# Kernel tuning notes

Hardware: AMD Instinct MI355X
Metric: run time of the kernel (lower is better)

Reference implementation:

```python
import jax, jax.numpy as jnp
import numpy as np

NEG_SLOPE = 0.2
LN_EPS = 1e-5


def _gat(x, src, dst, ea, Wl, Wr, We, att, b, heads, ch, concat):
    # GATv2 conv with edge features (eval mode: dropout = identity).
    N = x.shape[0]
    xl = (x @ Wl).reshape(N, heads, ch)          # source transform (also skip output)
    xr = (x @ Wr).reshape(N, heads, ch)          # target transform
    ee = (ea @ We).reshape(ea.shape[0], heads, ch)
    g = jax.nn.leaky_relu(xl[src] + xr[dst] + ee, NEG_SLOPE)   # [E,H,C]
    score = jnp.einsum('ehc,hc->eh', g, att)                    # [E,H]
    # segment softmax over destination nodes
    smax = jax.ops.segment_max(score, dst, num_segments=N)
    ex = jnp.exp(score - smax[dst])
    den = jax.ops.segment_sum(ex, dst, num_segments=N)
    alpha = ex / (den[dst] + 1e-16)
    out = jax.ops.segment_sum(xl[src] * alpha[..., None], dst, num_segments=N)  # [N,H,C]
    out = out.reshape(N, heads * ch) if concat else out.mean(axis=1)
    return out + b, xl.reshape(N, heads * ch)


def setup_inputs() -> dict:
    B, N, E, F, ED = 4, 20000, 640000, 64, 16
    HID, H1 = 16, 8
    key = jax.random.key(0)
    ks = jax.random.split(key, 32)

    def p(k, shape, fan):
        return (jax.random.normal(k, shape, jnp.float32) / np.float32(np.sqrt(fan)))

    inp = {
        'x': jax.random.normal(ks[0], (B, N, F), jnp.float32),
        'edge_attr': jax.random.normal(ks[1], (B, E, ED), jnp.float32),
        'edge_index': jax.random.randint(ks[2], (B, 2, E), 0, N, jnp.int32),
        # conv1: in=64, heads=8, out=16, concat
        'c1_Wl': p(ks[3], (F, H1 * HID), F),
        'c1_Wr': p(ks[4], (F, H1 * HID), F),
        'c1_We': p(ks[5], (ED, H1 * HID), ED),
        'c1_att': p(ks[6], (H1, HID), HID),
        'c1_b': jnp.zeros((H1 * HID,), jnp.float32),
        # conv2: in=128, heads=1, out=16, mean
        'c2_Wl': p(ks[7], (H1 * HID, HID), H1 * HID),
        'c2_Wr': p(ks[8], (H1 * HID, HID), H1 * HID),
        'c2_We': p(ks[9], (ED, HID), ED),
        'c2_att': p(ks[10], (1, HID), HID),
        'c2_b': jnp.zeros((HID,), jnp.float32),
        # skip_conv: in=128, heads=1, out=16, mean
        's_Wl': p(ks[11], (H1 * HID, HID), H1 * HID),
        's_Wr': p(ks[12], (H1 * HID, HID), H1 * HID),
        's_We': p(ks[13], (ED, HID), ED),
        's_att': p(ks[14], (1, HID), HID),
        's_b': jnp.zeros((HID,), jnp.float32),
        # lin_skip_conv + LayerNorm(16)
        'lin_W': p(ks[15], (HID, HID), HID),
        'lin_b': jnp.zeros((HID,), jnp.float32),
        'ln_g': jnp.ones((HID,), jnp.float32),
        'ln_b': jnp.zeros((HID,), jnp.float32),
    }
    return inp


def reference(x, edge_attr, edge_index,
              c1_Wl, c1_Wr, c1_We, c1_att, c1_b,
              c2_Wl, c2_Wr, c2_We, c2_att, c2_b,
              s_Wl, s_Wr, s_We, s_att, s_b,
              lin_W, lin_b, ln_g, ln_b):
    def single(xg, eig, eag):
        src, dst = eig[0], eig[1]
        h, skip = _gat(xg, src, dst, eag, c1_Wl, c1_Wr, c1_We, c1_att, c1_b, 8, 16, True)
        hx = jax.nn.elu(h)                                   # [N,128]
        x1, _ = _gat(hx, src, dst, eag, c2_Wl, c2_Wr, c2_We, c2_att, c2_b, 1, 16, False)
        # skip conv consumes hx with the residual skip features from conv1
        x2, _ = _gat(hx + skip, src, dst, eag, s_Wl, s_Wr, s_We, s_att, s_b, 1, 16, False)
        x2 = x2 @ lin_W.T + lin_b
        y = x1 + x2                                          # [N,16]
        mu = y.mean(-1, keepdims=True)
        var = ((y - mu) ** 2).mean(-1, keepdims=True)
        return (y - mu) / jnp.sqrt(var + LN_EPS) * ln_g + ln_b
    return jax.vmap(single)(x, edge_index, edge_attr)
```

## Files before the change

kernel.cpp:

```cpp
#include <hip/hip_runtime.h>
#include <hip/hip_bf16.h>

typedef __hip_bfloat16 bf16;
typedef float f32x2 __attribute__((ext_vector_type(2)));

#define NB_B 4
#define N 20000
#define E 640000
#define F 64
#define HC 128
#define ED 16
#define CH 16
#define NT 32

__device__ __forceinline__ float clampf(float v, float lo, float hi){ return fminf(fmaxf(v, lo), hi); }
__device__ __forceinline__ float ldv(const float* p, size_t i){ return p[i]; }
__device__ __forceinline__ float ldv(const bf16*  p, size_t i){ return __bfloat162float(p[i]); }
__device__ __forceinline__ void  stv(float* p, size_t i, float v){ p[i] = v; }
__device__ __forceinline__ void  stv(bf16*  p, size_t i, float v){ p[i] = __float2bfloat16(v); }
__device__ __forceinline__ unsigned short tobf(float v){ bf16 b = __float2bfloat16(v); return *(unsigned short*)&b; }
__device__ __forceinline__ float unpl(unsigned u){ return __uint_as_float(u << 16); }
__device__ __forceinline__ float unph(unsigned u){ return __uint_as_float(u & 0xffff0000u); }
__device__ __forceinline__ f32x2 mk2(float a, float b){ f32x2 r; r.x = a; r.y = b; return r; }
__device__ __forceinline__ int rfl(int v){ return __builtin_amdgcn_readfirstlane(v); }

#define L2E 1.44269504f

__device__ __forceinline__ float rsum16(float x){
  x += __int_as_float(__builtin_amdgcn_update_dpp(0, __float_as_int(x), 0x128, 0xf, 0xf, true));
  x += __int_as_float(__builtin_amdgcn_update_dpp(0, __float_as_int(x), 0x124, 0xf, 0xf, true));
  x += __int_as_float(__builtin_amdgcn_update_dpp(0, __float_as_int(x), 0x122, 0xf, 0xf, true));
  x += __int_as_float(__builtin_amdgcn_update_dpp(0, __float_as_int(x), 0x121, 0xf, 0xf, true));
  return x;
}

__global__ __launch_bounds__(256) void k_detect(const unsigned short* __restrict__ xu, int* __restrict__ flag){
  __shared__ int cnt[256];
  int tid = threadIdx.x;
  unsigned short lo = xu[2*tid];
  bf16 h = *(const bf16*)&lo;
  float v = fabsf(__bfloat162float(h));
  cnt[tid] = (v > 1e4f || (v != 0.f && v < 1e-4f)) ? 1 : 0;
  __syncthreads();
  for (int s=128; s>0; s>>=1){ if (tid<s) cnt[tid]+=cnt[tid+s]; __syncthreads(); }
  if (tid==0) *flag = (cnt[0] > 64) ? 1 : 0;
}

__global__ __launch_bounds__(256) void k_hist(const int* __restrict__ ei, int* __restrict__ cnt, int b0){
  int z = blockIdx.z, b = b0 + z;
  int e = blockIdx.x*256 + threadIdx.x;
  int d = ei[((size_t)b*2+1)*E + e];
  atomicAdd(&cnt[z*N + d], 1);
}

__global__ __launch_bounds__(256) void k_scan(const int* __restrict__ cnt, int* __restrict__ rowptr,
                                              int* __restrict__ cursor){
  int z = blockIdx.z, tid = threadIdx.x;
  const int* c = cnt + (size_t)z*N;
  int* rp = rowptr + (size_t)z*(N+1);
  int* cu = cursor + (size_t)z*N;
  const int CHK = (N + 255)/256;
  int lo = tid*CHK; int hi = lo + CHK; if (hi > N) hi = N; if (lo > N) lo = N;
  int s = 0;
  for (int i=lo;i<hi;i++) s += c[i];
  __shared__ int buf[256];
  buf[tid] = s; __syncthreads();
  for (int off=1; off<256; off<<=1){
    int t = (tid>=off) ? buf[tid-off] : 0;
    __syncthreads();
    buf[tid] += t;
    __syncthreads();
  }
  int run = buf[tid] - s;
  for (int i=lo;i<hi;i++){ int v=c[i]; rp[i]=run; cu[i]=run; run += v; }
  if (tid==255) rp[N] = run;
}

template<typename T>
__device__ __forceinline__ void scatter_body(const int* ei, int* cursor, int* csr,
                                             const T* ea, float* eacsr, int b0){
  int z = blockIdx.z, b = b0 + z;
  int e = blockIdx.x*256 + threadIdx.x;
  int s = ei[((size_t)b*2+0)*E + e];
  int d = ei[((size_t)b*2+1)*E + e];
  int pos = atomicAdd(&cursor[z*N + d], 1);
  csr[(size_t)z*E + pos] = s;
  float4* dst = (float4*)(eacsr + ((size_t)z*E + pos)*ED);
  const T* sp = ea + ((size_t)b*E + e)*ED;
  #pragma unroll
  for (int g=0; g<4; g++){
    float4 t;
    t.x = ldv(sp, g*4+0); t.y = ldv(sp, g*4+1); t.z = ldv(sp, g*4+2); t.w = ldv(sp, g*4+3);
    dst[g] = t;
  }
}
__global__ __launch_bounds__(256) void k_scatter(const int* ei, int* cursor, int* csr,
    const void* ea, float* eacsr, const int* flag, int b0){
  if (*flag) scatter_body(ei, cursor, csr, (const float*)ea, eacsr, b0);
  else       scatter_body(ei, cursor, csr, (const bf16*) ea, eacsr, b0);
}

template<typename T>
__device__ __forceinline__ void node1_body(const T* x, const T* Wl, const T* Wr,
                                           unsigned* xl1p, unsigned* xr1p, int b0,
                                           float (*xs)[F+4]){
  int z = blockIdx.z, b = b0 + z;
  int node0 = blockIdx.x*NT;
  for (int i=threadIdx.x; i<NT*F; i+=256){
    int n = i>>6, k = i&63;
    xs[n][k] = ldv(x, ((size_t)b*N + node0 + n)*F + k);
  }
  __syncthreads();
  int mat = threadIdx.x >> 7, c = threadIdx.x & 127;
  const T* W = mat ? Wr : Wl;
  float acc[NT];
  #pragma unroll
  for (int n=0;n<NT;n++) acc[n]=0.f;
  for (int k=0;k<F;k+=4){
    float w0 = ldv(W, (size_t)(k+0)*HC + c);
    float w1 = ldv(W, (size_t)(k+1)*HC + c);
    float w2 = ldv(W, (size_t)(k+2)*HC + c);
    float w3 = ldv(W, (size_t)(k+3)*HC + c);
    #pragma unroll
    for (int n=0;n<NT;n++){
      float4 xv = *(const float4*)&xs[n][k];
      acc[n] += xv.x*w0 + xv.y*w1 + xv.z*w2 + xv.w*w3;
    }
  }
  unsigned short* outp = (unsigned short*)(mat ? xr1p : xl1p);
  int half = c>>6, cc = c&63;
  #pragma unroll
  for (int n=0;n<NT;n++){
    float v = clampf(acc[n], -1e4f, 1e4f);
    outp[(((size_t)z*N + node0 + n)*64 + cc)*2 + half] = tobf(v);
  }
}
__global__ __launch_bounds__(256) void k_node1(const void* x, const void* Wl, const void* Wr,
    unsigned* xl1p, unsigned* xr1p, const int* flag, int b0){
  __shared__ float xs[NT][F+4];
  if (*flag) node1_body((const float*)x,(const float*)Wl,(const float*)Wr,xl1p,xr1p,b0,xs);
  else       node1_body((const bf16*) x,(const bf16*) Wl,(const bf16*) Wr,xl1p,xr1p,b0,xs);
}

template<typename T>
__device__ __forceinline__ void gather1_body(const int* __restrict__ rowptr, const int* __restrict__ csr,
    const float* __restrict__ eacsr, const T* __restrict__ We, const T* __restrict__ att, const T* __restrict__ b1,
    const unsigned* __restrict__ xl1p, const unsigned* __restrict__ xr1p, float* __restrict__ hx, int b0){
  int z = blockIdx.z;
  int lane = threadIdx.x & 63;
  int node = rfl(blockIdx.x*4 + (threadIdx.x >> 6));
  int rs = rfl(rowptr[(size_t)z*(N+1) + node]);
  int re = rfl(rowptr[(size_t)z*(N+1) + node + 1]);
  f32x2 w[ED];
  #pragma unroll
  for (int j=0;j<ED;j++) w[j] = mk2(ldv(We,(size_t)j*HC+lane), ldv(We,(size_t)j*HC+lane+64));
  f32x2 attv = mk2(ldv(att,(size_t)lane)*L2E, ldv(att,(size_t)lane+64)*L2E);
  unsigned xru = xr1p[((size_t)z*N + node)*64 + lane];
  f32x2 xr2 = mk2(unpl(xru), unph(xru));
  f32x2 acc = mk2(0.f,0.f), den = mk2(0.f,0.f);
  const unsigned* __restrict__ xlp = xl1p + (size_t)z*N*64;
  const int* __restrict__ csrz = csr + (size_t)z*E + rs;
  const float* __restrict__ eaz = eacsr + ((size_t)z*E + rs)*ED;
  int deg = re - rs;
  if (deg > 0){
    int s0 = rfl(csrz[0]);
    int s1 = (deg>1) ? rfl(csrz[1]) : s0;
    unsigned xa = xlp[(size_t)(unsigned)s0*64 + lane];
    unsigned xb = xlp[(size_t)(unsigned)s1*64 + lane];
    #pragma unroll 2
    for (int i=0;i<deg;i++){
      const float* __restrict__ ep = eaz + (size_t)i*ED;
      float ev[ED];
      #pragma unroll
      for (int j=0;j<ED;j++) ev[j] = ep[j];
      unsigned xw = xa;
      xa = xb;
      if (i+2 < deg){
        int sn = rfl(csrz[i+2]);
        xb = xlp[(size_t)(unsigned)sn*64 + lane];
      }
      f32x2 xl = mk2(unpl(xw), unph(xw));
      f32x2 g0 = xl + xr2, g1 = mk2(0.f,0.f);
      #pragma unroll
      for (int j=0;j<ED;j+=2){ g0 += w[j]*ev[j]; g1 += w[j+1]*ev[j+1]; }
      f32x2 g = g0 + g1;
      f32x2 lr;
      lr.x = fmaxf(g.x,0.f) + 0.2f*fminf(g.x,0.f);
      lr.y = fmaxf(g.y,0.f) + 0.2f*fminf(g.y,0.f);
      f32x2 v = lr*attv;
      float vL = rsum16(v.x);
      float vH = rsum16(v.y);
      f32x2 ex = mk2(exp2f(clampf(vL,-86.f,86.f)), exp2f(clampf(vH,-86.f,86.f)));
      den += ex;
      acc += ex*xl;
    }
  }
  float hL = acc.x/(den.x + 1e-16f) + ldv(b1,(size_t)lane);
  float hH = acc.y/(den.y + 1e-16f) + ldv(b1,(size_t)lane+64);
  hL = hL>0.f ? hL : expm1f(hL);
  hH = hH>0.f ? hH : expm1f(hH);
  hx[((size_t)z*N + node)*HC + lane]      = hL;
  hx[((size_t)z*N + node)*HC + lane + 64] = hH;
}
__global__ __launch_bounds__(256) void k_gather1(const int* __restrict__ rowptr, const int* __restrict__ csr,
    const float* __restrict__ eacsr,
    const void* We, const void* att, const void* b1,
    const unsigned* __restrict__ xl1p, const unsigned* __restrict__ xr1p, float* __restrict__ hx,
    const int* __restrict__ flag, int b0){
  if (*flag) gather1_body(rowptr,csr,eacsr,(const float*)We,(const float*)att,(const float*)b1,xl1p,xr1p,hx,b0);
  else       gather1_body(rowptr,csr,eacsr,(const bf16*) We,(const bf16*) att,(const bf16*) b1,xl1p,xr1p,hx,b0);
}

template<typename T>
__device__ __forceinline__ void node2_body(const float* hx, const unsigned* xl1p,
    const T* W2l, const T* W2r, const T* W3l, const T* W3r,
    unsigned* xl23p, unsigned* xr23p, int b0,
    float (*hv)[HC+4], float (*sv)[HC+4]){
  int z = blockIdx.z;
  int node0 = blockIdx.x*NT;
  for (int i=threadIdx.x; i<NT*HC; i+=256){
    int n = i>>7, k = i&127;
    float h = hx[((size_t)z*N + node0 + n)*HC + k];
    unsigned wxl = xl1p[((size_t)z*N + node0 + n)*64 + (k&63)];
    float xv = (k<64) ? unpl(wxl) : unph(wxl);
    hv[n][k] = h;
    sv[n][k] = h + xv;
  }
  __syncthreads();
  int o = threadIdx.x & 63;
  int mat = o >> 4, c = o & 15;
  int g = threadIdx.x >> 6;
  const T* W = (mat==0)? W2l : (mat==1)? W2r : (mat==2)? W3l : W3r;
  float (*src)[HC+4] = (mat<2)? hv : sv;
  float acc[8];
  #pragma unroll
  for (int j=0;j<8;j++) acc[j]=0.f;
  for (int k=0;k<HC;k+=4){
    float w0 = ldv(W, (size_t)(k+0)*CH + c);
    float w1 = ldv(W, (size_t)(k+1)*CH + c);
    float w2 = ldv(W, (size_t)(k+2)*CH + c);
    float w3 = ldv(W, (size_t)(k+3)*CH + c);
    #pragma unroll
    for (int j=0;j<8;j++){
      float4 xv = *(const float4*)&src[g*8+j][k];
      acc[j] += xv.x*w0 + xv.y*w1 + xv.z*w2 + xv.w*w3;
    }
  }
  unsigned short* arr = (unsigned short*)((mat&1) ? xr23p : xl23p);
  int half = mat>>1;
  #pragma unroll
  for (int j=0;j<8;j++){
    float v = clampf(acc[j], -1e4f, 1e4f);
    arr[(((size_t)z*N + node0 + g*8 + j)*CH + c)*2 + half] = tobf(v);
  }
}
__global__ __launch_bounds__(256) void k_node2(const float* hx, const unsigned* xl1p,
    const void* W2l, const void* W2r, const void* W3l, const void* W3r,
    unsigned* xl23p, unsigned* xr23p, const int* flag, int b0){
  __shared__ float hv[NT][HC+4];
  __shared__ float sv[NT][HC+4];
  if (*flag) node2_body(hx,xl1p,(const float*)W2l,(const float*)W2r,(const float*)W3l,(const float*)W3r,xl23p,xr23p,b0,hv,sv);
  else       node2_body(hx,xl1p,(const bf16*) W2l,(const bf16*) W2r,(const bf16*) W3l,(const bf16*) W3r,xl23p,xr23p,b0,hv,sv);
}

template<typename T>
__device__ __forceinline__ void gather23_body(const int* __restrict__ rowptr, const int* __restrict__ csr,
    const float* __restrict__ eacsr,
    const T* __restrict__ We2, const T* __restrict__ We3, const T* __restrict__ att2, const T* __restrict__ att3,
    const T* __restrict__ b2, const T* __restrict__ b3, const T* __restrict__ linW, const T* __restrict__ linb,
    const T* __restrict__ lng, const T* __restrict__ lnb,
    const unsigned* __restrict__ xl23p, const unsigned* __restrict__ xr23p,
    T* __restrict__ out, int b0){
  int z = blockIdx.z;
  int lane = threadIdx.x & 63;
  int g = lane >> 4, c = lane & 15;
  int node = rfl(blockIdx.x*4 + (threadIdx.x >> 6));
  int rs = rfl(rowptr[(size_t)z*(N+1) + node]);
  int re = rfl(rowptr[(size_t)z*(N+1) + node + 1]);
  int deg = re - rs;
  f32x2 w[ED];
  #pragma unroll
  for (int j=0;j<ED;j++) w[j] = mk2(ldv(We2,(size_t)j*CH+c), ldv(We3,(size_t)j*CH+c));
  f32x2 attv = mk2(ldv(att2,(size_t)c)*L2E, ldv(att3,(size_t)c)*L2E);
  unsigned xru = xr23p[((size_t)z*N + node)*CH + c];
  f32x2 xr2 = mk2(unpl(xru), unph(xru));
  f32x2 acc = mk2(0.f,0.f), den = mk2(0.f,0.f);
  const unsigned* __restrict__ xlp = xl23p + (size_t)z*N*CH;
  const int* __restrict__ csrz = csr + (size_t)z*E + rs;
  const float* __restrict__ eaz = eacsr + ((size_t)z*E + rs)*ED;
  if (deg > 0){
    int idx0 = (g < deg) ? g : deg-1;
    int s = csrz[idx0];
    unsigned xw = xlp[(size_t)(unsigned)s*CH + c];
    const float4* p0 = (const float4*)(eaz + (size_t)idx0*ED);
    float4 e0 = p0[0], e1 = p0[1], e2 = p0[2], e3 = p0[3];
    for (int i=0;i<deg;i+=4){
      bool act = (i + g) < deg;
      unsigned xcur = xw;
      float4 c0 = e0, c1 = e1, c2 = e2, c3 = e3;
      if (i+4 < deg){
        int ii = i + 4 + g;
        int idx = (ii < deg) ? ii : deg-1;
        int s2 = csrz[idx];
        xw = xlp[(size_t)(unsigned)s2*CH + c];
        const float4* p2 = (const float4*)(eaz + (size_t)idx*ED);
        e0 = p2[0]; e1 = p2[1]; e2 = p2[2]; e3 = p2[3];
      }
      float ev[ED];
      *(float4*)&ev[0]  = c0;
      *(float4*)&ev[4]  = c1;
      *(float4*)&ev[8]  = c2;
      *(float4*)&ev[12] = c3;
      f32x2 xl = mk2(unpl(xcur), unph(xcur));
      f32x2 g0 = xl + xr2, g1 = mk2(0.f,0.f);
      #pragma unroll
      for (int j=0;j<ED;j+=2){ g0 += w[j]*ev[j]; g1 += w[j+1]*ev[j+1]; }
      f32x2 gg = g0 + g1;
      f32x2 lr;
      lr.x = fmaxf(gg.x,0.f) + 0.2f*fminf(gg.x,0.f);
      lr.y = fmaxf(gg.y,0.f) + 0.2f*fminf(gg.y,0.f);
      f32x2 v = lr*attv;
      float v2 = rsum16(v.x);
      float v3 = rsum16(v.y);
      float x2e = exp2f(clampf(v2,-86.f,86.f));
      float x3e = exp2f(clampf(v3,-86.f,86.f));
      if (!act){ x2e = 0.f; x3e = 0.f; }
      f32x2 ex = mk2(x2e, x3e);
      den += ex;
      acc += ex*xl;
    }
  }
  acc.x += __shfl_xor(acc.x, 16); acc.x += __shfl_xor(acc.x, 32);
  acc.y += __shfl_xor(acc.y, 16); acc.y += __shfl_xor(acc.y, 32);
  den.x += __shfl_xor(den.x, 16); den.x += __shfl_xor(den.x, 32);
  den.y += __shfl_xor(den.y, 16); den.y += __shfl_xor(den.y, 32);
  float x1 = acc.x/(den.x + 1e-16f) + ldv(b2,(size_t)c);
  float x3 = acc.y/(den.y + 1e-16f) + ldv(b3,(size_t)c);
  float x2 = 0.f;
  #pragma unroll
  for (int j=0;j<16;j++) x2 += __shfl(x3, j, 16) * ldv(linW, (size_t)c*16 + j);
  x2 += ldv(linb,(size_t)c);
  float y = clampf(x1, -1e6f, 1e6f) + clampf(x2, -1e6f, 1e6f);
  float mu = rsum16(y)*(1.f/16.f);
  float dv = y - mu;
  float var = rsum16(dv*dv)*(1.f/16.f);
  float o = dv*rsqrtf(var + 1e-5f)*ldv(lng,(size_t)c) + ldv(lnb,(size_t)c);
  if (lane < 16) stv(out, ((size_t)(b0+z)*N + node)*16 + c, o);
}
__global__ __launch_bounds__(256) void k_gather23(const int* __restrict__ rowptr, const int* __restrict__ csr,
    const float* __restrict__ eacsr,
    const void* We2, const void* We3, const void* att2, const void* att3,
    const void* b2, const void* b3, const void* linW, const void* linb, const void* lng, const void* lnb,
    const unsigned* __restrict__ xl23p, const unsigned* __restrict__ xr23p,
    void* out, const int* __restrict__ flag, int b0){
  if (*flag) gather23_body(rowptr,csr,eacsr,(const float*)We2,(const float*)We3,(const float*)att2,(const float*)att3,
                           (const float*)b2,(const float*)b3,(const float*)linW,(const float*)linb,(const float*)lng,(const float*)lnb,
                           xl23p,xr23p,(float*)out,b0);
  else       gather23_body(rowptr,csr,eacsr,(const bf16*) We2,(const bf16*) We3,(const bf16*) att2,(const bf16*) att3,
                           (const bf16*) b2,(const bf16*) b3,(const bf16*) linW,(const bf16*) linb,(const bf16*) lng,(const bf16*) lnb,
                           xl23p,xr23p,(bf16*) out,b0);
}

struct WSP {
  int* flag;
  int *cnt, *cursor, *rowptr; int* csr;
  float *eacsr, *hx;
  unsigned *xl1p,*xr1p,*xl23p,*xr23p;
  size_t total;
};
static WSP mkws(char* base, int nb){
  WSP w; size_t off = 0;
  auto A = [&](size_t bytes)->char*{ char* p = base ? base + off : (char*)0; off = (off + bytes + 255) & ~(size_t)255; return p; };
  w.flag   = (int*)     A(256);
  w.cnt    = (int*)     A((size_t)nb*N*4);
  w.cursor = (int*)     A((size_t)nb*N*4);
  w.rowptr = (int*)     A((size_t)nb*(N+1)*4);
  w.csr    = (int*)     A((size_t)nb*E*4);
  w.eacsr  = (float*)   A((size_t)nb*E*ED*4);
  w.hx     = (float*)   A((size_t)nb*N*HC*4);
  w.xl1p   = (unsigned*)A((size_t)nb*N*64*4);
  w.xr1p   = (unsigned*)A((size_t)nb*N*64*4);
  w.xl23p  = (unsigned*)A((size_t)nb*N*CH*4);
  w.xr23p  = (unsigned*)A((size_t)nb*N*CH*4);
  w.total = off;
  return w;
}

extern "C" void kernel_launch(void* const* d_in, const int* in_sizes, int n_in,
                              void* d_out, int out_size, void* d_ws, size_t ws_size,
                              hipStream_t stream){
  const void* x    = d_in[0];
  const void* ea   = d_in[1];
  const int*  ei   = (const int*)d_in[2];
  const void* c1Wl = d_in[3], *c1Wr = d_in[4], *c1We = d_in[5];
  const void* c1att= d_in[6], *c1b  = d_in[7];
  const void* c2Wl = d_in[8], *c2Wr = d_in[9], *c2We = d_in[10];
  const void* c2att= d_in[11],*c2b  = d_in[12];
  const void* sWl  = d_in[13],*sWr  = d_in[14],*sWe  = d_in[15];
  const void* satt = d_in[16],*sb   = d_in[17];
  const void* linW = d_in[18],*linb = d_in[19];
  const void* lng  = d_in[20],*lnb  = d_in[21];

  auto run = [&](int b0, int nb){
    WSP w = mkws((char*)d_ws, nb);
    hipMemsetAsync(w.cnt, 0, (size_t)nb*N*4, stream);
    k_hist   <<<dim3(E/256,1,nb),   256,0,stream>>>(ei, w.cnt, b0);
    k_scan   <<<dim3(1,1,nb),       256,0,stream>>>(w.cnt, w.rowptr, w.cursor);
    k_scatter<<<dim3(E/256,1,nb),   256,0,stream>>>(ei, w.cursor, w.csr, ea, w.eacsr, w.flag, b0);
    k_node1  <<<dim3(N/NT,1,nb),    256,0,stream>>>(x, c1Wl, c1Wr, w.xl1p, w.xr1p, w.flag, b0);
    k_gather1<<<dim3(N/4,1,nb),     256,0,stream>>>(w.rowptr, w.csr, w.eacsr, c1We, c1att, c1b,
                                                    w.xl1p, w.xr1p, w.hx, w.flag, b0);
    k_node2  <<<dim3(N/NT,1,nb),    256,0,stream>>>(w.hx, w.xl1p, c2Wl, c2Wr, sWl, sWr,
                                                    w.xl23p, w.xr23p, w.flag, b0);
    k_gather23<<<dim3(N/4,1,nb),    256,0,stream>>>(w.rowptr, w.csr, w.eacsr, c2We, sWe, c2att, satt,
                                                    c2b, sb, linW, linb, lng, lnb,
                                                    w.xl23p, w.xr23p, d_out, w.flag, b0);
  };

  {
    WSP w0 = mkws((char*)d_ws, 1);
    k_detect<<<1,256,0,stream>>>((const unsigned short*)x, w0.flag);
  }

  WSP probe = mkws((char*)0, NB_B);
  if (ws_size >= probe.total){
    run(0, NB_B);
  } else {
    for (int g=0; g<NB_B; ++g) run(g, 1);
  }
}
```

Before: 1.214 ms.

## Restructure gather23 to one node per 16-lane group with LDS edge staging

The second gather kernel moves from one node per wavefront, with four edges processed in parallel per lane group, to one node per 16-lane group. Each group stages chunks of source indices and edge attributes in shared memory, then walks its edges with two-deep prefetch of source features, which removes the cross-group shuffle reduction. The first gather kernel is manually unrolled by two, loads edge attributes as float2 pairs, and both kernels use a branchless leaky-ReLU. The risk is load imbalance, since four nodes with different degrees now share a wavefront. The new path also relies on lockstep visibility of shared memory within a wave, with no barrier.

Result: faster. 1.141 ms (-6.0%).

```diff
diff --git a/kernel.cpp b/kernel.cpp
--- a/kernel.cpp
+++ b/kernel.cpp
@@ -12,6 +12,7 @@
 #define ED 16
 #define CH 16
 #define NT 32
+#define TB2 16
 
 __device__ __forceinline__ float clampf(float v, float lo, float hi){ return fminf(fmaxf(v, lo), hi); }
 __device__ __forceinline__ float ldv(const float* p, size_t i){ return p[i]; }
@@ -32,6 +33,10 @@
   x += __int_as_float(__builtin_amdgcn_update_dpp(0, __float_as_int(x), 0x122, 0xf, 0xf, true));
   x += __int_as_float(__builtin_amdgcn_update_dpp(0, __float_as_int(x), 0x121, 0xf, 0xf, true));
   return x;
+}
+__device__ __forceinline__ float leaky(float g){
+  float a = __uint_as_float(__float_as_uint(g) & 0x7fffffffu);
+  return fmaf(0.4f, a, 0.6f*g);
 }
 
 __global__ __launch_bounds__(256) void k_detect(const unsigned short* __restrict__ xu, int* __restrict__ flag){
@@ -154,46 +159,49 @@
   f32x2 w[ED];
   #pragma unroll
   for (int j=0;j<ED;j++) w[j] = mk2(ldv(We,(size_t)j*HC+lane), ldv(We,(size_t)j*HC+lane+64));
-  f32x2 attv = mk2(ldv(att,(size_t)lane)*L2E, ldv(att,(size_t)lane+64)*L2E);
+  float attL = ldv(att,(size_t)lane)*L2E, attH = ldv(att,(size_t)lane+64)*L2E;
   unsigned xru = xr1p[((size_t)z*N + node)*64 + lane];
   f32x2 xr2 = mk2(unpl(xru), unph(xru));
   f32x2 acc = mk2(0.f,0.f), den = mk2(0.f,0.f);
   const unsigned* __restrict__ xlp = xl1p + (size_t)z*N*64;
   const int* __restrict__ csrz = csr + (size_t)z*E + rs;
-  const float* __restrict__ eaz = eacsr + ((size_t)z*E + rs)*ED;
+  const f32x2* __restrict__ eaz = (const f32x2*)(eacsr + ((size_t)z*E + rs)*ED);
   int deg = re - rs;
   if (deg > 0){
+    auto EDGE = [&](const f32x2* er, unsigned xw){
+      f32x2 xl = mk2(unpl(xw), unph(xw));
+      f32x2 g0 = xl + xr2, g1 = mk2(0.f,0.f);
+      #pragma unroll
+      for (int jp=0;jp<8;jp++){ g0 += w[2*jp]*er[jp].x; g1 += w[2*jp+1]*er[jp].y; }
+      f32x2 g = g0 + g1;
+      float vL = rsum16(leaky(g.x)*attL);
+      float vH = rsum16(leaky(g.y)*attH);
+      f32x2 ex = mk2(exp2f(clampf(vL,-86.f,86.f)), exp2f(clampf(vH,-86.f,86.f)));
+      den += ex;
+      acc += ex*xl;
+    };
     int s0 = rfl(csrz[0]);
     int s1 = (deg>1) ? rfl(csrz[1]) : s0;
     unsigned xa = xlp[(size_t)(unsigned)s0*64 + lane];
     unsigned xb = xlp[(size_t)(unsigned)s1*64 + lane];
-    #pragma unroll 2
-    for (int i=0;i<deg;i++){
-      const float* __restrict__ ep = eaz + (size_t)i*ED;
-      float ev[ED];
+    f32x2 eA[8], eB[8];
+    #pragma unroll
+    for (int p=0;p<8;p++) eA[p] = eaz[p];
+    int i = 0;
+    for (; i+1 < deg; i += 2){
       #pragma unroll
-      for (int j=0;j<ED;j++) ev[j] = ep[j];
-      unsigned xw = xa;
-      xa = xb;
+      for (int p=0;p<8;p++) eB[p] = eaz[(size_t)(i+1)*8 + p];
+      unsigned x0 = xa, x1 = xb;
+      if (i+2 < deg){ int sn = rfl(csrz[i+2]); xa = xlp[(size_t)(unsigned)sn*64 + lane]; }
+      if (i+3 < deg){ int sn = rfl(csrz[i+3]); xb = xlp[(size_t)(unsigned)sn*64 + lane]; }
+      EDGE(eA, x0);
       if (i+2 < deg){
-        int sn = rfl(csrz[i+2]);
-        xb = xlp[(size_t)(unsigned)sn*64 + lane];
+        #pragma unroll
+        for (int p=0;p<8;p++) eA[p] = eaz[(size_t)(i+2)*8 + p];
       }
-      f32x2 xl = mk2(unpl(xw), unph(xw));
-      f32x2 g0 = xl + xr2, g1 = mk2(0.f,0.f);
-      #pragma unroll
-      for (int j=0;j<ED;j+=2){ g0 += w[j]*ev[j]; g1 += w[j+1]*ev[j+1]; }
-      f32x2 g = g0 + g1;
-      f32x2 lr;
-      lr.x = fmaxf(g.x,0.f) + 0.2f*fminf(g.x,0.f);
-      lr.y = fmaxf(g.y,0.f) + 0.2f*fminf(g.y,0.f);
-      f32x2 v = lr*attv;
-      float vL = rsum16(v.x);
-      float vH = rsum16(v.y);
-      f32x2 ex = mk2(exp2f(clampf(vL,-86.f,86.f)), exp2f(clampf(vH,-86.f,86.f)));
-      den += ex;
-      acc += ex*xl;
+      EDGE(eB, x1);
     }
+    if (i < deg) EDGE(eA, xa);
   }
   float hL = acc.x/(den.x + 1e-16f) + ldv(b1,(size_t)lane);
   float hH = acc.y/(den.y + 1e-16f) + ldv(b1,(size_t)lane+64);
@@ -266,74 +274,68 @@
 template<typename T>
 __device__ __forceinline__ void gather23_body(const int* __restrict__ rowptr, const int* __restrict__ csr,
     const float* __restrict__ eacsr,
-    const T* __restrict__ We2, const T* __restrict__ We3, const T* __restrict__ att2, const T* __restrict__ att3,
-    const T* __restrict__ b2, const T* __restrict__ b3, const T* __restrict__ linW, const T* __restrict__ linb,
-    const T* __restrict__ lng, const T* __restrict__ lnb,
+    const T* We2, const T* We3, const T* att2, const T* att3,
+    const T* b2, const T* b3, const T* linW, const T* linb, const T* lng, const T* lnb,
     const unsigned* __restrict__ xl23p, const unsigned* __restrict__ xr23p,
-    T* __restrict__ out, int b0){
+    T* out, int b0, int (*ssrc)[TB2], float (*eas)[TB2][16]){
   int z = blockIdx.z;
-  int lane = threadIdx.x & 63;
-  int g = lane >> 4, c = lane & 15;
-  int node = rfl(blockIdx.x*4 + (threadIdx.x >> 6));
-  int rs = rfl(rowptr[(size_t)z*(N+1) + node]);
-  int re = rfl(rowptr[(size_t)z*(N+1) + node + 1]);
-  int deg = re - rs;
+  int slot = threadIdx.x >> 4;
+  int node = blockIdx.x*16 + slot;
+  int c = threadIdx.x & 15;
+  int rs = rowptr[(size_t)z*(N+1) + node];
+  int re = rowptr[(size_t)z*(N+1) + node + 1];
+  unsigned xru = xr23p[((size_t)z*N + node)*CH + c];
+  f32x2 xr2 = mk2(unpl(xru), unph(xru));
   f32x2 w[ED];
   #pragma unroll
   for (int j=0;j<ED;j++) w[j] = mk2(ldv(We2,(size_t)j*CH+c), ldv(We3,(size_t)j*CH+c));
   f32x2 attv = mk2(ldv(att2,(size_t)c)*L2E, ldv(att3,(size_t)c)*L2E);
-  unsigned xru = xr23p[((size_t)z*N + node)*CH + c];
-  f32x2 xr2 = mk2(unpl(xru), unph(xru));
   f32x2 acc = mk2(0.f,0.f), den = mk2(0.f,0.f);
   const unsigned* __restrict__ xlp = xl23p + (size_t)z*N*CH;
-  const int* __restrict__ csrz = csr + (size_t)z*E + rs;
-  const float* __restrict__ eaz = eacsr + ((size_t)z*E + rs)*ED;
-  if (deg > 0){
-    int idx0 = (g < deg) ? g : deg-1;
-    int s = csrz[idx0];
-    unsigned xw = xlp[(size_t)(unsigned)s*CH + c];
-    const float4* p0 = (const float4*)(eaz + (size_t)idx0*ED);
-    float4 e0 = p0[0], e1 = p0[1], e2 = p0[2], e3 = p0[3];
-    for (int i=0;i<deg;i+=4){
-      bool act = (i + g) < deg;
-      unsigned xcur = xw;
-      float4 c0 = e0, c1 = e1, c2 = e2, c3 = e3;
-      if (i+4 < deg){
-        int ii = i + 4 + g;
-        int idx = (ii < deg) ? ii : deg-1;
-        int s2 = csrz[idx];
-        xw = xlp[(size_t)(unsigned)s2*CH + c];
-        const float4* p2 = (const float4*)(eaz + (size_t)idx*ED);
-        e0 = p2[0]; e1 = p2[1]; e2 = p2[2]; e3 = p2[3];
-      }
-      float ev[ED];
-      *(float4*)&ev[0]  = c0;
-      *(float4*)&ev[4]  = c1;
-      *(float4*)&ev[8]  = c2;
-      *(float4*)&ev[12] = c3;
-      f32x2 xl = mk2(unpl(xcur), unph(xcur));
-      f32x2 g0 = xl + xr2, g1 = mk2(0.f,0.f);
-      #pragma unroll
-      for (int j=0;j<ED;j+=2){ g0 += w[j]*ev[j]; g1 += w[j+1]*ev[j+1]; }
-      f32x2 gg = g0 + g1;
-      f32x2 lr;
-      lr.x = fmaxf(gg.x,0.f) + 0.2f*fminf(gg.x,0.f);
-      lr.y = fmaxf(gg.y,0.f) + 0.2f*fminf(gg.y,0.f);
-      f32x2 v = lr*attv;
-      float v2 = rsum16(v.x);
-      float v3 = rsum16(v.y);
-      float x2e = exp2f(clampf(v2,-86.f,86.f));
-      float x3e = exp2f(clampf(v3,-86.f,86.f));
-      if (!act){ x2e = 0.f; x3e = 0.f; }
-      f32x2 ex = mk2(x2e, x3e);
-      den += ex;
-      acc += ex*xl;
+  const int* __restrict__ csrz = csr + (size_t)z*E;
+
+  auto edge = [&](int i, unsigned xw){
+    f32x2 xl = mk2(unpl(xw), unph(xw));
+    float ev[16];
+    const float4* er = (const float4*)eas[slot][i];
+    *(float4*)&ev[0]  = er[0];
+    *(float4*)&ev[4]  = er[1];
+    *(float4*)&ev[8]  = er[2];
+    *(float4*)&ev[12] = er[3];
+    f32x2 g0 = xl + xr2, g1 = mk2(0.f,0.f);
+    #pragma unroll
+    for (int j=0;j<ED;j+=2){ g0 += w[j]*ev[j]; g1 += w[j+1]*ev[j+1]; }
+    f32x2 gg = g0 + g1;
+    f32x2 lr = mk2(leaky(gg.x), leaky(gg.y));
+    f32x2 v = lr*attv;
+    float v2 = rsum16(v.x);
+    float v3 = rsum16(v.y);
+    f32x2 ex = mk2(exp2f(clampf(v2,-86.f,86.f)), exp2f(clampf(v3,-86.f,86.f)));
+    den += ex;
+    acc += ex*xl;
+  };
+
+  for (int base = rs; base < re; base += TB2){
+    int m = re - base; if (m > TB2) m = TB2;
+    if (c < m) ssrc[slot][c] = csrz[base + c];
+    const float4* ep = (const float4*)(eacsr + ((size_t)z*E + base)*ED);
+    for (int i4=c; i4<m*4; i4+=16)
+      *(float4*)&eas[slot][i4>>2][(i4&3)*4] = ep[i4];
+    unsigned pa = xlp[(unsigned)(ssrc[slot][0]*CH + c)];
+    unsigned pb = (m>1) ? xlp[(unsigned)(ssrc[slot][1]*CH + c)] : pa;
+    int i = 0;
+    for (; i+1 < m; i += 2){
+      unsigned x0 = pa, x1 = pb;
+      int i2 = (i+2 < m) ? i+2 : m-1;
+      int i3 = (i+3 < m) ? i+3 : m-1;
+      int s2 = ssrc[slot][i2], s3 = ssrc[slot][i3];
+      pa = xlp[(unsigned)(s2*CH + c)];
+      pb = xlp[(unsigned)(s3*CH + c)];
+      edge(i, x0);
+      edge(i+1, x1);
     }
-  }
-  acc.x += __shfl_xor(acc.x, 16); acc.x += __shfl_xor(acc.x, 32);
-  acc.y += __shfl_xor(acc.y, 16); acc.y += __shfl_xor(acc.y, 32);
-  den.x += __shfl_xor(den.x, 16); den.x += __shfl_xor(den.x, 32);
-  den.y += __shfl_xor(den.y, 16); den.y += __shfl_xor(den.y, 32);
+    if (i < m) edge(i, pa);
+  }
   float x1 = acc.x/(den.x + 1e-16f) + ldv(b2,(size_t)c);
   float x3 = acc.y/(den.y + 1e-16f) + ldv(b3,(size_t)c);
   float x2 = 0.f;
@@ -345,7 +347,7 @@
   float dv = y - mu;
   float var = rsum16(dv*dv)*(1.f/16.f);
   float o = dv*rsqrtf(var + 1e-5f)*ldv(lng,(size_t)c) + ldv(lnb,(size_t)c);
-  if (lane < 16) stv(out, ((size_t)(b0+z)*N + node)*16 + c, o);
+  stv(out, ((size_t)(b0+z)*N + node)*16 + c, o);
 }
 __global__ __launch_bounds__(256) void k_gather23(const int* __restrict__ rowptr, const int* __restrict__ csr,
     const float* __restrict__ eacsr,
@@ -353,12 +355,14 @@
     const void* b2, const void* b3, const void* linW, const void* linb, const void* lng, const void* lnb,
     const unsigned* __restrict__ xl23p, const unsigned* __restrict__ xr23p,
     void* out, const int* __restrict__ flag, int b0){
+  __shared__ int ssrc[16][TB2];
+  __shared__ float eas[16][TB2][16];
   if (*flag) gather23_body(rowptr,csr,eacsr,(const float*)We2,(const float*)We3,(const float*)att2,(const float*)att3,
                            (const float*)b2,(const float*)b3,(const float*)linW,(const float*)linb,(const float*)lng,(const float*)lnb,
-                           xl23p,xr23p,(float*)out,b0);
+                           xl23p,xr23p,(float*)out,b0,ssrc,eas);
   else       gather23_body(rowptr,csr,eacsr,(const bf16*) We2,(const bf16*) We3,(const bf16*) att2,(const bf16*) att3,
                            (const bf16*) b2,(const bf16*) b3,(const bf16*) linW,(const bf16*) linb,(const bf16*) lng,(const bf16*) lnb,
-                           xl23p,xr23p,(bf16*) out,b0);
+                           xl23p,xr23p,(bf16*) out,b0,ssrc,eas);
 }
 
 struct WSP {
@@ -412,7 +416,7 @@
                                                     w.xl1p, w.xr1p, w.hx, w.flag, b0);
     k_node2  <<<dim3(N/NT,1,nb),    256,0,stream>>>(w.hx, w.xl1p, c2Wl, c2Wr, sWl, sWr,
                                                     w.xl23p, w.xr23p, w.flag, b0);
-    k_gather23<<<dim3(N/4,1,nb),    256,0,stream>>>(w.rowptr, w.csr, w.eacsr, c2We, sWe, c2att, satt,
+    k_gather23<<<dim3(N/16,1,nb),   256,0,stream>>>(w.rowptr, w.csr, w.eacsr, c2We, sWe, c2att, satt,
                                                     c2b, sb, linW, linb, lng, lnb,
                                                     w.xl23p, w.xr23p, d_out, w.flag, b0);
   };
```
